# Kernel tuning notes

Hardware: AMD Instinct MI355X
Metric: run time of the kernel (lower is better)

Reference implementation:

```python
import jax, jax.numpy as jnp
import numpy as np

N_HEAD = 50000
N_TAIL = 50000
E = 1600000
IN_F = 256
OUT_F = 32
NHEAD = 4
EDGE_F = 64
N_ETYPES = 5
NEG_SLOPE = 0.2


def setup_inputs() -> dict:
    key = jax.random.key(0)
    ks = jax.random.split(key, 10)
    return {
        "head_feature": jax.random.normal(ks[0], (N_HEAD, IN_F), jnp.float32),
        "tail_feature": jax.random.normal(ks[1], (N_TAIL, IN_F), jnp.float32),
        "W": jax.random.normal(ks[2], (IN_F, OUT_F * NHEAD), jnp.float32) * 0.05,
        "W_e": jax.random.normal(ks[3], (EDGE_F, EDGE_F * NHEAD), jnp.float32) * 0.05,
        "edge_emb": jax.random.normal(ks[4], (N_ETYPES, EDGE_F), jnp.float32) * 0.1,
        "a_l": jax.random.normal(ks[5], (1, NHEAD, OUT_F), jnp.float32) * 0.1,
        "a_r": jax.random.normal(ks[6], (1, NHEAD, OUT_F), jnp.float32) * 0.1,
        "a_e": jax.random.normal(ks[7], (1, NHEAD, EDGE_F), jnp.float32) * 0.1,
        "edge_list": jax.random.randint(ks[8], (2, E), 0, N_HEAD, jnp.int64),
        "tmp_edge": jax.random.randint(ks[9], (E,), 0, N_ETYPES, jnp.int64),
    }


def reference(head_feature, tail_feature, W, W_e, edge_emb, a_l, a_r, a_e, edge_list, tmp_edge):
    n_head_nodes = head_feature.shape[0]
    nhead, out_dim = a_l.shape[1], a_l.shape[2]
    edge_feats = a_e.shape[2]

    # dense projections (dropout in eval mode = identity)
    h_head = (head_feature @ W).reshape(-1, nhead, out_dim)   # [Nh, H, D]
    h_tail = (tail_feature @ W).reshape(-1, nhead, out_dim)   # [Nt, H, D]
    e = (edge_emb @ W_e).reshape(-1, nhead, edge_feats)       # [T,  H, De]

    head_ind = edge_list[0]
    tail_ind = edge_list[1]

    # per-edge attention logits [E, H]
    h_e = (a_e * e).sum(-1)[tmp_edge]
    h_l = (a_l * h_head).sum(-1)[head_ind]
    h_r = (a_r * h_tail).sum(-1)[tail_ind]
    att = jax.nn.leaky_relu(h_l + h_r + h_e, negative_slope=NEG_SLOPE)

    # sparse softmax over dim=1 (per head-node row), per head
    m = jax.ops.segment_max(att, head_ind, num_segments=n_head_nodes)
    m = jnp.where(jnp.isfinite(m), m, jnp.zeros_like(m))  # empty rows
    ex = jnp.exp(att - m[head_ind])
    denom = jax.ops.segment_sum(ex, head_ind, num_segments=n_head_nodes)
    alpha = ex / denom[head_ind]                              # [E, H]

    # sparse-mm aggregation: out[i] = sum_e alpha_e * h_tail[tail_e]
    msg = alpha[..., None] * h_tail[tail_ind]                 # [E, H, D]
    out = jax.ops.segment_sum(msg, head_ind, num_segments=n_head_nodes)
    out = out.reshape(n_head_nodes, nhead * out_dim)
    out = jax.nn.elu(out)
    return out, alpha
```

## Files before the change

kernel.cpp:

```cpp
#include <hip/hip_runtime.h>
#include <hip/hip_bf16.h>
#include <string.h>

#define NNODE 50000
#define NEDGE 1600000
#define INF   256
#define NH    4
#define EF    64
#define NET   5

#define NBUCK 782
#define BCAP  2560
#define EPB   2048
#define PBLK  782
#define RDB   1563

typedef unsigned short u16t;
typedef __attribute__((ext_vector_type(8))) short short8;
typedef __attribute__((ext_vector_type(4))) float f32x4;

__device__ __forceinline__ float b2f(u16t u) {
    union { unsigned int i; float f; } v; v.i = ((unsigned int)u) << 16; return v.f;
}
__device__ __forceinline__ u16t f2b(float f) {
    __hip_bfloat16 h = __float2bfloat16(f);
    u16t u; memcpy(&u, &h, 2); return u;
}

__global__ void k_detect(const int* __restrict__ el, const int* __restrict__ ety,
                         int* __restrict__ flag) {
    int tid = threadIdx.x;
    int w = tid >> 6, lane = tid & 63;
    const int* p = (w == 0) ? el : ety;
    int x = p[2 * lane + 1];
    unsigned long long b = __ballot(x != 0);
    if (lane == 0) flag[w] = (b == 0ULL) ? 1 : 0;
}

__global__ void k_prep(const float* __restrict__ W, const float* __restrict__ We,
                       const float* __restrict__ emb, const float* __restrict__ al,
                       const float* __restrict__ ar, const float* __restrict__ ae,
                       float* __restrict__ wl, float* __restrict__ wr,
                       float* __restrict__ he) {
    __shared__ float wes[EF * NH];
    int tid = threadIdx.x;
    {
        int k = tid;
        for (int h = 0; h < NH; h++) {
            float accl = 0.f, accr = 0.f;
            for (int d = 0; d < 32; d++) {
                float w = W[k * 128 + h * 32 + d];
                accl += w * al[h * 32 + d];
                accr += w * ar[h * 32 + d];
            }
            wl[k * NH + h] = accl;
            wr[k * NH + h] = accr;
        }
    }
    if (tid < EF) {
        int k = tid;
        for (int h = 0; h < NH; h++) {
            float s = 0.f;
            for (int d = 0; d < EF; d++)
                s += We[k * (NH * EF) + h * EF + d] * ae[h * EF + d];
            wes[k * NH + h] = s;
        }
    }
    __syncthreads();
    if (tid < NET * NH) {
        int t = tid / NH, h = tid % NH;
        float s = 0.f;
        for (int k = 0; k < EF; k++)
            s += emb[t * EF + k] * wes[k * NH + h];
        he[tid] = s;
    }
}

__global__ void k_prepw(const float* __restrict__ W, u16t* __restrict__ Wfrag) {
    int idx = blockIdx.x * 256 + threadIdx.x;
    int j    = idx & 7;
    int lane = (idx >> 3) & 63;
    int ks   = (idx >> 9) & 7;
    int tile = idx >> 12;
    int n = tile * 16 + (lane & 15);
    int k = ks * 32 + (lane >> 4) * 8 + j;
    Wfrag[idx] = f2b(W[k * 128 + n]);
}

__global__ void k_fuseA(const float* __restrict__ head, const float* __restrict__ tail,
                        const float* __restrict__ wl, const float* __restrict__ wr,
                        const int* __restrict__ el, const int* __restrict__ ety,
                        const int* __restrict__ flag, int* __restrict__ cursor,
                        unsigned int* __restrict__ bucketbuf,
                        float* __restrict__ hl, float* __restrict__ hr) {
    __shared__ unsigned int srec[EPB];
    __shared__ u16t sbuck[EPB];
    __shared__ int hist[784];
    __shared__ int loff[784];
    __shared__ int gb[784];
    __shared__ int psum[256];
    int b = blockIdx.x;
    int tid = threadIdx.x;
    if (b < PBLK) {
        int base = b * EPB;
        int wf = flag[0], wt = flag[1];
        for (int i = tid; i < 784; i += 256) hist[i] = 0;
        __syncthreads();
        unsigned int rec[8];
        unsigned int br[8];
#pragma unroll
        for (int i = 0; i < 8; i++) {
            int e = base + i * 256 + tid;
            br[i] = 0xffffffffu;
            rec[i] = 0;
            if (e < NEDGE) {
                int hi = wf ? el[2 * (long long)e]           : el[e];
                int ti = wf ? el[2 * ((long long)NEDGE + e)] : el[NEDGE + e];
                int ty = wt ? ety[2 * (long long)e]          : ety[e];
                int bk = hi >> 6;
                int r = atomicAdd(&hist[bk], 1);
                rec[i] = (unsigned)ti | ((unsigned)(hi & 63) << 16) | ((unsigned)ty << 22);
                br[i]  = (unsigned)bk | ((unsigned)r << 16);
            }
        }
        __syncthreads();
        int s4[4]; int tsum = 0;
        if (tid < 196) {
#pragma unroll
            for (int j = 0; j < 4; j++) { s4[j] = hist[4 * tid + j]; tsum += s4[j]; }
        }
        psum[tid] = (tid < 196) ? tsum : 0;
        __syncthreads();
        for (int off = 1; off < 256; off <<= 1) {
            int v = (tid >= off) ? psum[tid - off] : 0;
            __syncthreads();
            psum[tid] += v;
            __syncthreads();
        }
        if (tid < 196) {
            int run = tid ? psum[tid - 1] : 0;
#pragma unroll
            for (int j = 0; j < 4; j++) {
                int bk = 4 * tid + j;
                loff[bk] = run;
                if (s4[j] > 0) gb[bk] = atomicAdd(&cursor[bk], s4[j]);
                run += s4[j];
            }
        }
        __syncthreads();
#pragma unroll
        for (int i = 0; i < 8; i++) {
            if (br[i] != 0xffffffffu) {
                int bk = br[i] & 0xffff;
                int r  = br[i] >> 16;
                int slot = loff[bk] + r;
                srec[slot] = rec[i];
                sbuck[slot] = (u16t)bk;
            }
        }
        __syncthreads();
        int tot = psum[255];
        for (int i = tid; i < tot; i += 256) {
            int bk = sbuck[i];
            int pos = gb[bk] + (i - loff[bk]);
            if (pos < BCAP) bucketbuf[(size_t)bk * BCAP + pos] = srec[i];
        }
    } else {
        int bb = b - PBLK;
        int ishead = (bb < RDB);
        const float* X  = ishead ? head : tail;
        const float* wv = ishead ? wl : wr;
        float* o        = ishead ? hl : hr;
        int rowbase = (ishead ? bb : bb - RDB) * 32;
        int wave = tid >> 6;
        int g = (tid >> 4) & 3;
        int l = tid & 15;
        const float4* wv4 = (const float4*)wv;
        float4 acc[2];
#pragma unroll
        for (int rr = 0; rr < 2; rr++) {
            acc[rr].x = 0.f; acc[rr].y = 0.f; acc[rr].z = 0.f; acc[rr].w = 0.f;
            int row = rowbase + rr * 16 + wave * 4 + g;
            if (row < NNODE) {
                const float* xp = X + (size_t)row * INF + l * 4;
#pragma unroll
                for (int c = 0; c < 4; c++) {
                    float4 xv = *(const float4*)(xp + c * 64);
                    float xs[4] = {xv.x, xv.y, xv.z, xv.w};
#pragma unroll
                    for (int j = 0; j < 4; j++) {
                        float4 wvv = wv4[c * 64 + l * 4 + j];
                        acc[rr].x += xs[j] * wvv.x;
                        acc[rr].y += xs[j] * wvv.y;
                        acc[rr].z += xs[j] * wvv.z;
                        acc[rr].w += xs[j] * wvv.w;
                    }
                }
            }
        }
#pragma unroll
        for (int rr = 0; rr < 2; rr++) {
#pragma unroll
            for (int off = 8; off > 0; off >>= 1) {
                acc[rr].x += __shfl_xor(acc[rr].x, off);
                acc[rr].y += __shfl_xor(acc[rr].y, off);
                acc[rr].z += __shfl_xor(acc[rr].z, off);
                acc[rr].w += __shfl_xor(acc[rr].w, off);
            }
            int row = rowbase + rr * 16 + wave * 4 + g;
            if (l == 0 && row < NNODE) ((float4*)o)[row] = acc[rr];
        }
    }
}

__global__ void k_bscan(const int* __restrict__ cursor, int* __restrict__ bstart,
                        int* __restrict__ row_start) {
    __shared__ int psum[256];
    int tid = threadIdx.x;
    int s4[4]; int tsum = 0;
    if (tid < 196) {
#pragma unroll
        for (int j = 0; j < 4; j++) {
            int bk = 4 * tid + j;
            s4[j] = (bk < NBUCK) ? cursor[bk] : 0;
            tsum += s4[j];
        }
    }
    psum[tid] = (tid < 196) ? tsum : 0;
    __syncthreads();
    for (int off = 1; off < 256; off <<= 1) {
        int v = (tid >= off) ? psum[tid - off] : 0;
        __syncthreads();
        psum[tid] += v;
        __syncthreads();
    }
    if (tid < 196) {
        int run = tid ? psum[tid - 1] : 0;
#pragma unroll
        for (int j = 0; j < 4; j++) {
            int bk = 4 * tid + j;
            if (bk < NBUCK) bstart[bk] = run;
            run += s4[j];
        }
    }
    if (tid == 255) {
        bstart[NBUCK] = psum[255];
        row_start[NNODE] = psum[255];
    }
}

__global__ void k_fuseB(const float* __restrict__ X, const u16t* __restrict__ Wfrag,
                        u16t* __restrict__ H, const unsigned int* __restrict__ bucketbuf,
                        const int* __restrict__ cursor, const int* __restrict__ bstart,
                        unsigned int* __restrict__ cpack, int* __restrict__ row_start) {
    __shared__ __attribute__((aligned(16))) u16t alds[16 * 264];
    __shared__ unsigned int lrec[BCAP];
    __shared__ unsigned int lord[BCAP];
    __shared__ int cnt[64];
    __shared__ int sc[64];
    int b = blockIdx.x;
    int tid = threadIdx.x;
    if (b < 3125) {
        int rowbase = b * 16;
        for (int i = tid; i < 1024; i += 256) {
            int row = i >> 6;
            int kc = (i & 63) * 4;
            float4 v = *(const float4*)(X + (size_t)(rowbase + row) * INF + kc);
            u16t* d = alds + row * 264 + kc;
            d[0] = f2b(v.x); d[1] = f2b(v.y); d[2] = f2b(v.z); d[3] = f2b(v.w);
        }
        __syncthreads();
        int wave = tid >> 6, lane = tid & 63;
        int m = lane & 15, quad = lane >> 4;
        int t0 = wave * 2, t1 = t0 + 1;
        f32x4 acc0 = {0.f, 0.f, 0.f, 0.f};
        f32x4 acc1 = {0.f, 0.f, 0.f, 0.f};
#pragma unroll
        for (int ks = 0; ks < 8; ks++) {
            short8 a  = *(const short8*)(alds + m * 264 + ks * 32 + quad * 8);
            short8 b0 = *(const short8*)(Wfrag + (((t0 * 8 + ks) * 64 + lane) << 3));
            short8 b1 = *(const short8*)(Wfrag + (((t1 * 8 + ks) * 64 + lane) << 3));
            acc0 = __builtin_amdgcn_mfma_f32_16x16x32_bf16(a, b0, acc0, 0, 0, 0);
            acc1 = __builtin_amdgcn_mfma_f32_16x16x32_bf16(a, b1, acc1, 0, 0, 0);
        }
        u16t* Hp = H + (size_t)rowbase * 128;
#pragma unroll
        for (int r = 0; r < 4; r++) {
            int row = quad * 4 + r;
            Hp[(size_t)row * 128 + t0 * 16 + m] = f2b(acc0[r]);
            Hp[(size_t)row * 128 + t1 * 16 + m] = f2b(acc1[r]);
        }
    } else {
        int q = b - 3125;
        int nrec = cursor[q];
        if (nrec > BCAP) nrec = BCAP;
        int bs = bstart[q];
        for (int i = tid; i < nrec; i += 256)
            lrec[i] = bucketbuf[(size_t)q * BCAP + i];
        if (tid < 64) cnt[tid] = 0;
        __syncthreads();
        unsigned int myr[10];
        int k2 = 0;
        for (int i = tid; i < nrec; i += 256) {
            int n = (lrec[i] >> 16) & 63;
            myr[k2++] = atomicAdd(&cnt[n], 1);
        }
        __syncthreads();
        if (tid < 64) sc[tid] = cnt[tid];
        __syncthreads();
        for (int off = 1; off < 64; off <<= 1) {
            int v = (tid >= off && tid < 64) ? sc[tid - off] : 0;
            __syncthreads();
            if (tid < 64) sc[tid] += v;
            __syncthreads();
        }
        k2 = 0;
        for (int i = tid; i < nrec; i += 256) {
            unsigned int rc = lrec[i];
            int n  = (rc >> 16) & 63;
            int ti = rc & 0xffff;
            int ty = rc >> 22;
            int pos = (sc[n] - cnt[n]) + (int)myr[k2++];
            lord[pos] = ((unsigned)ty << 16) | (unsigned)ti;
        }
        __syncthreads();
        for (int i = tid; i < nrec; i += 256)
            cpack[bs + i] = lord[i];
        if (tid < 64) {
            int node = q * 64 + tid;
            if (node < NNODE) row_start[node] = bs + (sc[tid] - cnt[tid]);
        }
    }
}

__global__ void k_agg(const int* __restrict__ rs, const unsigned int* __restrict__ cpack,
                      const float* __restrict__ hl, const float* __restrict__ hr,
                      const float* __restrict__ heg, const u16t* __restrict__ ht,
                      float* __restrict__ den, float2* __restrict__ out) {
    __shared__ float hes[NET * NH];
    int tid = threadIdx.x;
    if (tid < NET * NH) hes[tid] = heg[tid];
    __syncthreads();
    int wave = tid >> 6, lane = tid & 63;
    int node = blockIdx.x * 4 + wave;
    int start = rs[node], end = rs[node + 1];
    int h = lane >> 4;
    float hlv = hl[node * 4 + h];
    float a0 = 0.f, a1 = 0.f, s = 0.f;
    int j = start;
    for (; j + 4 <= end; j += 4) {
        unsigned c0 = cpack[j], c1 = cpack[j + 1], c2 = cpack[j + 2], c3 = cpack[j + 3];
        int t0 = c0 & 0xffff, t1 = c1 & 0xffff, t2 = c2 & 0xffff, t3 = c3 & 0xffff;
        float r0 = hr[t0 * 4 + h], r1 = hr[t1 * 4 + h];
        float r2 = hr[t2 * 4 + h], r3 = hr[t3 * 4 + h];
        unsigned v0 = *(const unsigned*)(ht + (size_t)t0 * 128 + lane * 2);
        unsigned v1 = *(const unsigned*)(ht + (size_t)t1 * 128 + lane * 2);
        unsigned v2 = *(const unsigned*)(ht + (size_t)t2 * 128 + lane * 2);
        unsigned v3 = *(const unsigned*)(ht + (size_t)t3 * 128 + lane * 2);
        float x0 = hlv + r0 + hes[(c0 >> 16) * 4 + h];
        float x1 = hlv + r1 + hes[(c1 >> 16) * 4 + h];
        float x2 = hlv + r2 + hes[(c2 >> 16) * 4 + h];
        float x3 = hlv + r3 + hes[(c3 >> 16) * 4 + h];
        x0 = x0 > 0.f ? x0 : 0.2f * x0;
        x1 = x1 > 0.f ? x1 : 0.2f * x1;
        x2 = x2 > 0.f ? x2 : 0.2f * x2;
        x3 = x3 > 0.f ? x3 : 0.2f * x3;
        float e0 = __expf(x0), e1 = __expf(x1), e2 = __expf(x2), e3 = __expf(x3);
        a0 += e0 * b2f((u16t)(v0 & 0xffff)) + e1 * b2f((u16t)(v1 & 0xffff))
            + e2 * b2f((u16t)(v2 & 0xffff)) + e3 * b2f((u16t)(v3 & 0xffff));
        a1 += e0 * b2f((u16t)(v0 >> 16)) + e1 * b2f((u16t)(v1 >> 16))
            + e2 * b2f((u16t)(v2 >> 16)) + e3 * b2f((u16t)(v3 >> 16));
        s  += e0 + e1 + e2 + e3;
    }
    for (; j < end; j++) {
        unsigned cp = cpack[j];
        int ti = cp & 0xffff;
        int ty = cp >> 16;
        float att = hlv + hr[ti * 4 + h] + hes[ty * 4 + h];
        att = att > 0.f ? att : 0.2f * att;
        float exv = __expf(att);
        unsigned int hv = *(const unsigned*)(ht + (size_t)ti * 128 + lane * 2);
        a0 += exv * b2f((u16t)(hv & 0xffff));
        a1 += exv * b2f((u16t)(hv >> 16));
        s  += exv;
    }
    if ((lane & 15) == 0) den[node * 4 + h] = s;
    float o0 = 0.f, o1 = 0.f;
    if (s > 0.f) { o0 = a0 / s; o1 = a1 / s; }
    o0 = o0 > 0.f ? o0 : expm1f(o0);
    o1 = o1 > 0.f ? o1 : expm1f(o1);
    float2 ov = {o0, o1};
    out[(size_t)node * 64 + lane] = ov;
}

__global__ void k_alpha(const int* __restrict__ el, const int* __restrict__ ety,
                        const int* __restrict__ flag,
                        const float* __restrict__ hl, const float* __restrict__ hr,
                        const float* __restrict__ heg, const float* __restrict__ den,
                        float* __restrict__ alpha) {
    __shared__ float hes[NET * NH];
    int tid = threadIdx.x;
    if (tid < NET * NH) hes[tid] = heg[tid];
    __syncthreads();
    int wf = flag[0], wt = flag[1];
    int e = blockIdx.x * 256 + tid;
    int hi = wf ? el[2 * (long long)e]           : el[e];
    int ti = wf ? el[2 * ((long long)NEDGE + e)] : el[NEDGE + e];
    int ty = wt ? ety[2 * (long long)e]          : ety[e];
    float4 l = ((const float4*)hl)[hi];
    float4 r = ((const float4*)hr)[ti];
    float4 d = ((const float4*)den)[hi];
    float v0 = l.x + r.x + hes[ty * 4 + 0];
    float v1 = l.y + r.y + hes[ty * 4 + 1];
    float v2 = l.z + r.z + hes[ty * 4 + 2];
    float v3 = l.w + r.w + hes[ty * 4 + 3];
    v0 = v0 > 0.f ? v0 : 0.2f * v0;
    v1 = v1 > 0.f ? v1 : 0.2f * v1;
    v2 = v2 > 0.f ? v2 : 0.2f * v2;
    v3 = v3 > 0.f ? v3 : 0.2f * v3;
    float4 o;
    o.x = d.x > 0.f ? __expf(v0) / d.x : 0.f;
    o.y = d.y > 0.f ? __expf(v1) / d.y : 0.f;
    o.z = d.z > 0.f ? __expf(v2) / d.z : 0.f;
    o.w = d.w > 0.f ? __expf(v3) / d.w : 0.f;
    ((float4*)alpha)[e] = o;
}

extern "C" void kernel_launch(void* const* d_in, const int* in_sizes, int n_in,
                              void* d_out, int out_size, void* d_ws, size_t ws_size,
                              hipStream_t stream) {
    const float* head = (const float*)d_in[0];
    const float* tail = (const float*)d_in[1];
    const float* W    = (const float*)d_in[2];
    const float* We   = (const float*)d_in[3];
    const float* emb  = (const float*)d_in[4];
    const float* al   = (const float*)d_in[5];
    const float* ar   = (const float*)d_in[6];
    const float* ae   = (const float*)d_in[7];
    const int*   el   = (const int*)d_in[8];
    const int*   ety  = (const int*)d_in[9];

    float* ws = (float*)d_ws;
    float* hl       = ws;
    float* hr       = ws + 200000;
    float* wl       = ws + 400000;
    float* wr       = ws + 401024;
    float* heg      = ws + 402048;
    int*   flag     = (int*)(ws + 402080);
    int*   bstart   = (int*)(ws + 402096);
    int*   cursor   = (int*)(ws + 402880);
    float* den      = ws + 403664;
    int*   row_start= (int*)(ws + 603664);
    u16t*  Wfrag    = (u16t*)(ws + 653668);

    float* outp   = (float*)d_out;
    float* alphap = (float*)d_out + 6400000;
    u16t*         htail = (u16t*)alphap;
    unsigned int* cpack = (unsigned int*)(alphap + 3200000);
    unsigned int* bucketbuf = (unsigned int*)outp;

    (void)hipMemsetAsync(cursor, 0, NBUCK * sizeof(int), stream);

    k_detect<<<1, 128, 0, stream>>>(el, ety, flag);
    k_prep<<<1, 256, 0, stream>>>(W, We, emb, al, ar, ae, wl, wr, heg);
    k_prepw<<<128, 256, 0, stream>>>(W, Wfrag);
    k_fuseA<<<PBLK + 2 * RDB, 256, 0, stream>>>(head, tail, wl, wr, el, ety, flag,
                                                cursor, bucketbuf, hl, hr);
    k_bscan<<<1, 256, 0, stream>>>(cursor, bstart, row_start);
    k_fuseB<<<3125 + NBUCK, 256, 0, stream>>>(tail, Wfrag, htail, bucketbuf,
                                              cursor, bstart, cpack, row_start);
    k_agg<<<NNODE / 4, 256, 0, stream>>>(row_start, cpack, hl, hr, heg, htail,
                                         den, (float2*)outp);
    k_alpha<<<NEDGE / 256, 256, 0, stream>>>(el, ety, flag, hl, hr, heg, den, alphap);
}
```

Baseline: 375.5 us.

## Replace global atomic bucket scatter with per-block histograms and gather

Partition blocks no longer use global atomics on bucket cursors and scattered writes. Each block now writes its locally sorted records contiguously, along with a per-block histogram and offset table. A new reduction kernel sums the histograms into bucket counts. The bucket consumer gathers its records from every partition block through a prefix scan. This removes atomic contention and scattered global writes in exchange for an extra kernel, extra 2D count/offset traffic, and a serial per-thread gather loop that reads many small, noncontiguous runs.

```diff
diff --git a/kernel.cpp b/kernel.cpp
--- a/kernel.cpp
+++ b/kernel.cpp
@@ -13,6 +13,7 @@
 #define BCAP  2560
 #define EPB   2048
 #define PBLK  782
+#define BKS   784
 #define RDB   1563
 
 typedef unsigned short u16t;
@@ -90,21 +91,20 @@
 __global__ void k_fuseA(const float* __restrict__ head, const float* __restrict__ tail,
                         const float* __restrict__ wl, const float* __restrict__ wr,
                         const int* __restrict__ el, const int* __restrict__ ety,
-                        const int* __restrict__ flag, int* __restrict__ cursor,
+                        const int* __restrict__ flag,
+                        int* __restrict__ hist2d, int* __restrict__ loff2d,
                         unsigned int* __restrict__ bucketbuf,
                         float* __restrict__ hl, float* __restrict__ hr) {
     __shared__ unsigned int srec[EPB];
-    __shared__ u16t sbuck[EPB];
-    __shared__ int hist[784];
-    __shared__ int loff[784];
-    __shared__ int gb[784];
+    __shared__ int hist[BKS];
+    __shared__ int loff[BKS];
     __shared__ int psum[256];
     int b = blockIdx.x;
     int tid = threadIdx.x;
     if (b < PBLK) {
         int base = b * EPB;
         int wf = flag[0], wt = flag[1];
-        for (int i = tid; i < 784; i += 256) hist[i] = 0;
+        for (int i = tid; i < BKS; i += 256) hist[i] = 0;
         __syncthreads();
         unsigned int rec[8];
         unsigned int br[8];
@@ -143,7 +143,8 @@
             for (int j = 0; j < 4; j++) {
                 int bk = 4 * tid + j;
                 loff[bk] = run;
-                if (s4[j] > 0) gb[bk] = atomicAdd(&cursor[bk], s4[j]);
+                hist2d[b * BKS + bk] = s4[j];
+                loff2d[b * BKS + bk] = run;
                 run += s4[j];
             }
         }
@@ -153,18 +154,13 @@
             if (br[i] != 0xffffffffu) {
                 int bk = br[i] & 0xffff;
                 int r  = br[i] >> 16;
-                int slot = loff[bk] + r;
-                srec[slot] = rec[i];
-                sbuck[slot] = (u16t)bk;
+                srec[loff[bk] + r] = rec[i];
             }
         }
         __syncthreads();
         int tot = psum[255];
-        for (int i = tid; i < tot; i += 256) {
-            int bk = sbuck[i];
-            int pos = gb[bk] + (i - loff[bk]);
-            if (pos < BCAP) bucketbuf[(size_t)bk * BCAP + pos] = srec[i];
-        }
+        for (int i = tid; i < tot; i += 256)
+            bucketbuf[(size_t)b * EPB + i] = srec[i];
     } else {
         int bb = b - PBLK;
         int ishead = (bb < RDB);
@@ -213,6 +209,21 @@
     }
 }
 
+__global__ void k_bsum(const int* __restrict__ hist2d, int* __restrict__ cursor) {
+    __shared__ int red[256];
+    int bk = blockIdx.x;
+    int tid = threadIdx.x;
+    int s = 0;
+    for (int sb = tid; sb < PBLK; sb += 256) s += hist2d[sb * BKS + bk];
+    red[tid] = s;
+    __syncthreads();
+    for (int off = 128; off > 0; off >>= 1) {
+        if (tid < off) red[tid] += red[tid + off];
+        __syncthreads();
+    }
+    if (tid == 0) cursor[bk] = red[0];
+}
+
 __global__ void k_bscan(const int* __restrict__ cursor, int* __restrict__ bstart,
                         int* __restrict__ row_start) {
     __shared__ int psum[256];
@@ -251,11 +262,13 @@
 
 __global__ void k_fuseB(const float* __restrict__ X, const u16t* __restrict__ Wfrag,
                         u16t* __restrict__ H, const unsigned int* __restrict__ bucketbuf,
-                        const int* __restrict__ cursor, const int* __restrict__ bstart,
+                        const int* __restrict__ hist2d, const int* __restrict__ loff2d,
+                        const int* __restrict__ bstart,
                         unsigned int* __restrict__ cpack, int* __restrict__ row_start) {
     __shared__ __attribute__((aligned(16))) u16t alds[16 * 264];
     __shared__ unsigned int lrec[BCAP];
     __shared__ unsigned int lord[BCAP];
+    __shared__ int psum[256];
     __shared__ int cnt[64];
     __shared__ int sc[64];
     int b = blockIdx.x;
@@ -292,13 +305,45 @@
         }
     } else {
         int q = b - 3125;
-        int nrec = cursor[q];
+        int bs = bstart[q];
+        int c4[4], o4[4]; int tsum = 0;
+        if (tid < 196) {
+#pragma unroll
+            for (int j = 0; j < 4; j++) {
+                int sb = 4 * tid + j;
+                c4[j] = 0; o4[j] = 0;
+                if (sb < PBLK) {
+                    c4[j] = hist2d[sb * BKS + q];
+                    o4[j] = loff2d[sb * BKS + q];
+                }
+                tsum += c4[j];
+            }
+        }
+        psum[tid] = (tid < 196) ? tsum : 0;
+        __syncthreads();
+        for (int off = 1; off < 256; off <<= 1) {
+            int v = (tid >= off) ? psum[tid - off] : 0;
+            __syncthreads();
+            psum[tid] += v;
+            __syncthreads();
+        }
+        if (tid < 196) {
+            int run = tid ? psum[tid - 1] : 0;
+#pragma unroll
+            for (int j = 0; j < 4; j++) {
+                int sb = 4 * tid + j;
+                for (int k = 0; k < c4[j]; k++) {
+                    int d = run + k;
+                    if (d < BCAP)
+                        lrec[d] = bucketbuf[(size_t)sb * EPB + o4[j] + k];
+                }
+                run += c4[j];
+            }
+        }
+        if (tid < 64) cnt[tid] = 0;
+        __syncthreads();
+        int nrec = psum[255];
         if (nrec > BCAP) nrec = BCAP;
-        int bs = bstart[q];
-        for (int i = tid; i < nrec; i += 256)
-            lrec[i] = bucketbuf[(size_t)q * BCAP + i];
-        if (tid < 64) cnt[tid] = 0;
-        __syncthreads();
         unsigned int myr[10];
         int k2 = 0;
         for (int i = tid; i < nrec; i += 256) {
@@ -458,17 +503,18 @@
     u16t*         htail = (u16t*)alphap;
     unsigned int* cpack = (unsigned int*)(alphap + 3200000);
     unsigned int* bucketbuf = (unsigned int*)outp;
-
-    (void)hipMemsetAsync(cursor, 0, NBUCK * sizeof(int), stream);
+    int* hist2d = (int*)outp + 1601536;
+    int* loff2d = hist2d + 613088;
 
     k_detect<<<1, 128, 0, stream>>>(el, ety, flag);
     k_prep<<<1, 256, 0, stream>>>(W, We, emb, al, ar, ae, wl, wr, heg);
     k_prepw<<<128, 256, 0, stream>>>(W, Wfrag);
     k_fuseA<<<PBLK + 2 * RDB, 256, 0, stream>>>(head, tail, wl, wr, el, ety, flag,
-                                                cursor, bucketbuf, hl, hr);
+                                                hist2d, loff2d, bucketbuf, hl, hr);
+    k_bsum<<<NBUCK, 256, 0, stream>>>(hist2d, cursor);
     k_bscan<<<1, 256, 0, stream>>>(cursor, bstart, row_start);
     k_fuseB<<<3125 + NBUCK, 256, 0, stream>>>(tail, Wfrag, htail, bucketbuf,
-                                              cursor, bstart, cpack, row_start);
+                                              hist2d, loff2d, bstart, cpack, row_start);
     k_agg<<<NNODE / 4, 256, 0, stream>>>(row_start, cpack, hl, hr, heg, htail,
                                          den, (float2*)outp);
     k_alpha<<<NEDGE / 256, 256, 0, stream>>>(el, ety, flag, hl, hr, heg, den, alphap);
```

Measured after the change: 341.6 us. 9.0% less time.
